# Optimization experiments

Measured on AMD Instinct MI355X. Metric: run time of the kernel, lower is better.

The kernel has to match this reference:

```python
import jax, jax.numpy as jnp
import numpy as np

B, T, V, E, U = 256, 512, 20000, 128, 128


def setup_inputs() -> dict:
    key = jax.random.key(0)
    k = jax.random.split(key, 7)
    tokens = jax.random.randint(k[0], (B, T), 0, V)
    emb_table = jax.random.normal(k[1], (V, E), jnp.float32) * 0.05
    kernel = jax.random.normal(k[2], (E, 4 * U), jnp.float32) * 0.05
    recurrent_kernel = jax.random.normal(k[3], (U, 4 * U), jnp.float32) * 0.05
    # Keras default: unit_forget_bias -> forget-gate bias = 1, others 0 (gate order i,f,c,o)
    bias = jnp.concatenate([jnp.zeros(U), jnp.ones(U), jnp.zeros(2 * U)]).astype(jnp.float32)
    dense_w = jax.random.normal(k[4], (U, 1), jnp.float32) * 0.05
    dense_b = jnp.zeros((1,), jnp.float32)
    return {"tokens": tokens, "emb_table": emb_table, "kernel": kernel,
            "recurrent_kernel": recurrent_kernel, "bias": bias,
            "dense_w": dense_w, "dense_b": dense_b}


def reference(tokens, emb_table, kernel, recurrent_kernel, bias, dense_w, dense_b):
    # Embedding lookup: [B,T] -> [B,T,E]
    x = emb_table[tokens]
    # Precompute input projections for all timesteps: [B,T,4U]
    zx = jnp.einsum('bte,eg->btg', x, kernel) + bias

    def step(carry, z_t):
        h, c = carry
        z = z_t + h @ recurrent_kernel          # [B,4U]
        i, f, g, o = jnp.split(z, 4, axis=-1)   # Keras gate order i,f,c,o
        i = jax.nn.sigmoid(i)
        f = jax.nn.sigmoid(f)
        g = jnp.tanh(g)
        o = jax.nn.sigmoid(o)
        c = f * c + i * g
        h = o * jnp.tanh(c)
        return (h, c), None

    h0 = jnp.zeros((tokens.shape[0], U), zx.dtype)
    c0 = jnp.zeros((tokens.shape[0], U), zx.dtype)
    (h_final, _), _ = jax.lax.scan(step, (h0, c0), jnp.swapaxes(zx, 0, 1))
    # Dense sigmoid head: [B,1]
    return jax.nn.sigmoid(h_final @ dense_w + dense_b)
```

## Files before the change

### kernel.cpp

```cpp
#include <hip/hip_runtime.h>
#include <hip/hip_bf16.h>

#define BB 256
#define TT 512
#define VV 20000
#define EE 128
#define UU 128
#define G4 512

typedef _Float16 h2 __attribute__((ext_vector_type(2)));

__device__ __forceinline__ float sigmoid_f(float x) {
    float e = __expf(-x);
    return __builtin_amdgcn_rcpf(1.0f + e);
}
__device__ __forceinline__ float tanh_f(float x) {
    float e = __expf(2.0f * x);
    return 1.0f - 2.0f * __builtin_amdgcn_rcpf(e + 1.0f);
}

__device__ __forceinline__ int dpp_i(int v, int pat) {
    switch (pat) {
        case 0xB1: return __builtin_amdgcn_mov_dpp(v, 0xB1, 0xF, 0xF, true);
        case 0x4E: return __builtin_amdgcn_mov_dpp(v, 0x4E, 0xF, 0xF, true);
        case 0x00: return __builtin_amdgcn_mov_dpp(v, 0x00, 0xF, 0xF, true);
        case 0x55: return __builtin_amdgcn_mov_dpp(v, 0x55, 0xF, 0xF, true);
        case 0xAA: return __builtin_amdgcn_mov_dpp(v, 0xAA, 0xF, 0xF, true);
        default:   return __builtin_amdgcn_mov_dpp(v, 0xFF, 0xF, 0xF, true);
    }
}
__device__ __forceinline__ float dpp_f(float v, int pat) {
    return __int_as_float(dpp_i(__float_as_int(v), pat));
}
__device__ __forceinline__ h2 pk_add_dpp(h2 s, int pat) {
    int m = dpp_i(__builtin_bit_cast(int, s), pat);
    return s + __builtin_bit_cast(h2, m);
}

__global__ __launch_bounds__(512, 2) void proj_kernel(
    const float* __restrict__ emb, const float* __restrict__ wk,
    const float* __restrict__ bias, float* __restrict__ P2) {
    const int tid = threadIdx.x;
    const int g   = tid & 3;
    const int u   = tid >> 2;
    const int col = g * 128 + u;
    const int v0  = blockIdx.x * 16;

    __shared__ float elds[16 * EE];
    ((float4*)elds)[tid] = ((const float4*)(emb + (size_t)v0 * EE))[tid];
    __syncthreads();

    float bcol = bias[col];
    float acc[16];
#pragma unroll
    for (int r = 0; r < 16; ++r) acc[r] = bcol;

    const float4* elds4 = (const float4*)elds;
    for (int e0 = 0; e0 < EE; e0 += 4) {
        float k0 = wk[(e0 + 0) * G4 + col];
        float k1 = wk[(e0 + 1) * G4 + col];
        float k2 = wk[(e0 + 2) * G4 + col];
        float k3 = wk[(e0 + 3) * G4 + col];
#pragma unroll
        for (int r = 0; r < 16; ++r) {
            float4 ev = elds4[r * 32 + (e0 >> 2)];
            acc[r] = fmaf(ev.x, k0, acc[r]);
            acc[r] = fmaf(ev.y, k1, acc[r]);
            acc[r] = fmaf(ev.z, k2, acc[r]);
            acc[r] = fmaf(ev.w, k3, acc[r]);
        }
    }
#pragma unroll
    for (int r = 0; r < 16; ++r)
        P2[(size_t)(v0 + r) * G4 + tid] = acc[r];
}

__global__ __launch_bounds__(512) __attribute__((amdgpu_waves_per_eu(2, 2)))
void lstm_kernel(
    const int* __restrict__ tokens, const float* __restrict__ rk,
    const float* __restrict__ P2, const float* __restrict__ dense_w,
    const float* __restrict__ dense_b, float* __restrict__ out) {
    const int tid = threadIdx.x;
    const int u   = tid >> 2;
    const int q   = tid & 3;
    const int b   = blockIdx.x;

    __shared__ __align__(16) _Float16 hh[2][UU];
    __shared__ int   tokLDS[TT + 4];
    __shared__ float red[8];

    h2 wgt[4][16];
    const float* rkb = rk + (size_t)(32 * q) * G4;
#pragma unroll
    for (int g = 0; g < 4; ++g) {
        const int c = g * 128 + u;
#pragma unroll
        for (int p = 0; p < 16; ++p) {
            h2 hw;
            hw.x = (_Float16)rkb[(2 * p + 0) * G4 + c];
            hw.y = (_Float16)rkb[(2 * p + 1) * G4 + c];
            wgt[g][p] = hw;
        }
    }

    const int* trow = tokens + (size_t)b * TT;
    tokLDS[tid] = trow[tid];
    if (tid < 4) tokLDS[TT + tid] = trow[TT - 1];
    if (tid < UU) hh[0][tid] = (_Float16)0.f;

    const int pOff = 4 * u + q;
    float c_state = 0.f, hv = 0.f;
    float pf0 = P2[(size_t)trow[0] * G4 + pOff];
    float pf1 = P2[(size_t)trow[1] * G4 + pOff];
    __syncthreads();

    const h2 zzero = {(_Float16)0.f, (_Float16)0.f};

#define LSTEP(PAR, PF)                                                        \
    {                                                                         \
        int vtok = tokLDS[t + (PAR) + 2];                                     \
        float pcur = (PF);                               \
        (PF) = P2[(size_t)vtok * G4 + pOff];          \
        const int4* hrow = (const int4*)&hh[PAR][32 * q];                     \
        int4 hA = hrow[0], hB = hrow[1], hC = hrow[2], hD = hrow[3];          \
        h2 hr[16];                                                            \
        hr[0]  = __builtin_bit_cast(h2, hA.x);                                \
        hr[1]  = __builtin_bit_cast(h2, hA.y);                                \
        hr[2]  = __builtin_bit_cast(h2, hA.z);                                \
        hr[3]  = __builtin_bit_cast(h2, hA.w);                                \
        hr[4]  = __builtin_bit_cast(h2, hB.x);                                \
        hr[5]  = __builtin_bit_cast(h2, hB.y);                                \
        hr[6]  = __builtin_bit_cast(h2, hB.z);                                \
        hr[7]  = __builtin_bit_cast(h2, hB.w);                                \
        hr[8]  = __builtin_bit_cast(h2, hC.x);                                \
        hr[9]  = __builtin_bit_cast(h2, hC.y);                                \
        hr[10] = __builtin_bit_cast(h2, hC.z);                                \
        hr[11] = __builtin_bit_cast(h2, hC.w);                                \
        hr[12] = __builtin_bit_cast(h2, hD.x);                                \
        hr[13] = __builtin_bit_cast(h2, hD.y);                                \
        hr[14] = __builtin_bit_cast(h2, hD.z);                                \
        hr[15] = __builtin_bit_cast(h2, hD.w);                                \
              \
        h2 a0[4], a1[4];                                                      \
        _Pragma("unroll")                                                     \
        for (int g = 0; g < 4; ++g) { a0[g] = zzero; a1[g] = zzero; }         \
        _Pragma("unroll")                                                     \
        for (int p = 0; p < 16; p += 2) {                                     \
            _Pragma("unroll")                                                 \
            for (int g = 0; g < 4; ++g) {                                     \
                a0[g] = hr[p] * wgt[g][p] + a0[g];                            \
                a1[g] = hr[p + 1] * wgt[g][p + 1] + a1[g];                    \
            }                                                                 \
        }                                                                     \
         \
        h2 s0 = a0[0] + a1[0], s1 = a0[1] + a1[1];                            \
        h2 s2 = a0[2] + a1[2], s3 = a0[3] + a1[3];                            \
        s0 = pk_add_dpp(s0, 0xB1); s0 = pk_add_dpp(s0, 0x4E);                 \
        s1 = pk_add_dpp(s1, 0xB1); s1 = pk_add_dpp(s1, 0x4E);                 \
        s2 = pk_add_dpp(s2, 0xB1); s2 = pk_add_dpp(s2, 0x4E);                 \
        s3 = pk_add_dpp(s3, 0xB1); s3 = pk_add_dpp(s3, 0x4E);                 \
                 \
        int ilo = (q & 1) ? __builtin_bit_cast(int, s1)                       \
                          : __builtin_bit_cast(int, s0);                      \
        int ihi = (q & 1) ? __builtin_bit_cast(int, s3)                       \
                          : __builtin_bit_cast(int, s2);                      \
        h2 own  = __builtin_bit_cast(h2, (q & 2) ? ihi : ilo);                \
        float zq = (float)own.x + (float)own.y + pcur;                        \
        float xs = (q == 2) ? zq + zq : zq;                                   \
        float sg = sigmoid_f(xs);                                             \
        float av = (q == 2) ? fmaf(2.f, sg, -1.f) : sg;                       \
                                     \
        float ai = dpp_f(av, 0x00);                                           \
        float af_ = dpp_f(av, 0x55);                                          \
        float ag = dpp_f(av, 0xAA);                                           \
        float ao = dpp_f(av, 0xFF);                                           \
        c_state = fmaf(af_, c_state, ai * ag);                                \
        hv      = ao * tanh_f(c_state);                                       \
        if (q == 0) hh[(PAR) ^ 1][u] = (_Float16)hv;                          \
        asm volatile("s_waitcnt lgkmcnt(0)" ::: "memory");                    \
        __builtin_amdgcn_s_barrier();                                         \
    }

    for (int t = 0; t < TT; t += 2) {
        LSTEP(0, pf0)
        LSTEP(1, pf1)
    }
#undef LSTEP

    float val = (q == 0) ? hv * dense_w[u] : 0.f;
#pragma unroll
    for (int off = 32; off > 0; off >>= 1) val += __shfl_xor(val, off, 64);
    if ((tid & 63) == 0) red[tid >> 6] = val;
    __syncthreads();
    if (tid == 0) {
        float s = dense_b[0];
#pragma unroll
        for (int i = 0; i < 8; ++i) s += red[i];
        out[b] = sigmoid_f(s);
    }
}

extern "C" void kernel_launch(void* const* d_in, const int* in_sizes, int n_in,
                              void* d_out, int out_size, void* d_ws, size_t ws_size,
                              hipStream_t stream) {
    const int*   tokens = (const int*)  d_in[0];
    const float* emb    = (const float*)d_in[1];
    const float* wk     = (const float*)d_in[2];
    const float* rk     = (const float*)d_in[3];
    const float* bias   = (const float*)d_in[4];
    const float* dw     = (const float*)d_in[5];
    const float* db     = (const float*)d_in[6];
    float* out = (float*)d_out;
    float* P2  = (float*)d_ws;

    proj_kernel<<<VV / 16, 512, 0, stream>>>(emb, wk, bias, P2);
    lstm_kernel<<<BB, 512, 0, stream>>>(tokens, rk, P2, dw, db, out);
}
```

Baseline: 355.9 us.

## Give each thread a full K-column per gate, removing cross-lane DPP reduction

Repartitions the recurrent matvec so each thread owns all 128 input rows for its own gate column instead of a 32-row slice across all four gates. This removes the per-step DPP butterfly reduction and gate selection, replacing them with a local tree of packed fp16 adds, and uses inline-asm v_pk_fma_f16. In exchange each thread reads the entire h vector from LDS every step, four times more LDS traffic, and accumulates longer fp16 chains, which may affect precision.

```diff
diff --git a/kernel.cpp b/kernel.cpp
--- a/kernel.cpp
+++ b/kernel.cpp
@@ -19,22 +19,25 @@
     return 1.0f - 2.0f * __builtin_amdgcn_rcpf(e + 1.0f);
 }
 
-__device__ __forceinline__ int dpp_i(int v, int pat) {
+__device__ __forceinline__ h2 pk_fma(h2 a, h2 b, h2 c) {
+    int d, ia = __builtin_bit_cast(int, a), ib = __builtin_bit_cast(int, b),
+        ic = __builtin_bit_cast(int, c);
+    asm("v_pk_fma_f16 %0, %1, %2, %3" : "=v"(d) : "v"(ia), "v"(ib), "v"(ic));
+    return __builtin_bit_cast(h2, d);
+}
+__device__ __forceinline__ h2 pk_add(h2 a, h2 b) {
+    int d, ia = __builtin_bit_cast(int, a), ib = __builtin_bit_cast(int, b);
+    asm("v_pk_add_f16 %0, %1, %2" : "=v"(d) : "v"(ia), "v"(ib));
+    return __builtin_bit_cast(h2, d);
+}
+
+__device__ __forceinline__ float dpp_f(float v, int pat) {
     switch (pat) {
-        case 0xB1: return __builtin_amdgcn_mov_dpp(v, 0xB1, 0xF, 0xF, true);
-        case 0x4E: return __builtin_amdgcn_mov_dpp(v, 0x4E, 0xF, 0xF, true);
-        case 0x00: return __builtin_amdgcn_mov_dpp(v, 0x00, 0xF, 0xF, true);
-        case 0x55: return __builtin_amdgcn_mov_dpp(v, 0x55, 0xF, 0xF, true);
-        case 0xAA: return __builtin_amdgcn_mov_dpp(v, 0xAA, 0xF, 0xF, true);
-        default:   return __builtin_amdgcn_mov_dpp(v, 0xFF, 0xF, 0xF, true);
+        case 0x00: return __int_as_float(__builtin_amdgcn_mov_dpp(__float_as_int(v), 0x00, 0xF, 0xF, true));
+        case 0x55: return __int_as_float(__builtin_amdgcn_mov_dpp(__float_as_int(v), 0x55, 0xF, 0xF, true));
+        case 0xAA: return __int_as_float(__builtin_amdgcn_mov_dpp(__float_as_int(v), 0xAA, 0xF, 0xF, true));
+        default:   return __int_as_float(__builtin_amdgcn_mov_dpp(__float_as_int(v), 0xFF, 0xF, 0xF, true));
     }
-}
-__device__ __forceinline__ float dpp_f(float v, int pat) {
-    return __int_as_float(dpp_i(__float_as_int(v), pat));
-}
-__device__ __forceinline__ h2 pk_add_dpp(h2 s, int pat) {
-    int m = dpp_i(__builtin_bit_cast(int, s), pat);
-    return s + __builtin_bit_cast(h2, m);
 }
 
 __global__ __launch_bounds__(512, 2) void proj_kernel(
@@ -89,17 +92,15 @@
     __shared__ int   tokLDS[TT + 4];
     __shared__ float red[8];
 
-    h2 wgt[4][16];
-    const float* rkb = rk + (size_t)(32 * q) * G4;
+    h2 wgt[64];
+    {
+        const int c = q * 128 + u;
 #pragma unroll
-    for (int g = 0; g < 4; ++g) {
-        const int c = g * 128 + u;
-#pragma unroll
-        for (int p = 0; p < 16; ++p) {
+        for (int p = 0; p < 64; ++p) {
             h2 hw;
-            hw.x = (_Float16)rkb[(2 * p + 0) * G4 + c];
-            hw.y = (_Float16)rkb[(2 * p + 1) * G4 + c];
-            wgt[g][p] = hw;
+            hw.x = (_Float16)rk[(size_t)(2 * p + 0) * G4 + c];
+            hw.y = (_Float16)rk[(size_t)(2 * p + 1) * G4 + c];
+            wgt[p] = hw;
         }
     }
 
@@ -108,10 +109,10 @@
     if (tid < 4) tokLDS[TT + tid] = trow[TT - 1];
     if (tid < UU) hh[0][tid] = (_Float16)0.f;
 
-    const int pOff = 4 * u + q;
+    const float* Pcol = P2 + (size_t)(4 * u + q);
     float c_state = 0.f, hv = 0.f;
-    float pf0 = P2[(size_t)trow[0] * G4 + pOff];
-    float pf1 = P2[(size_t)trow[1] * G4 + pOff];
+    float pf0 = Pcol[(size_t)trow[0] * G4];
+    float pf1 = Pcol[(size_t)trow[1] * G4];
     __syncthreads();
 
     const h2 zzero = {(_Float16)0.f, (_Float16)0.f};
@@ -120,60 +121,40 @@
     {                                                                         \
         int vtok = tokLDS[t + (PAR) + 2];                                     \
         float pcur = (PF);                               \
-        (PF) = P2[(size_t)vtok * G4 + pOff];          \
-        const int4* hrow = (const int4*)&hh[PAR][32 * q];                     \
-        int4 hA = hrow[0], hB = hrow[1], hC = hrow[2], hD = hrow[3];          \
-        h2 hr[16];                                                            \
-        hr[0]  = __builtin_bit_cast(h2, hA.x);                                \
-        hr[1]  = __builtin_bit_cast(h2, hA.y);                                \
-        hr[2]  = __builtin_bit_cast(h2, hA.z);                                \
-        hr[3]  = __builtin_bit_cast(h2, hA.w);                                \
-        hr[4]  = __builtin_bit_cast(h2, hB.x);                                \
-        hr[5]  = __builtin_bit_cast(h2, hB.y);                                \
-        hr[6]  = __builtin_bit_cast(h2, hB.z);                                \
-        hr[7]  = __builtin_bit_cast(h2, hB.w);                                \
-        hr[8]  = __builtin_bit_cast(h2, hC.x);                                \
-        hr[9]  = __builtin_bit_cast(h2, hC.y);                                \
-        hr[10] = __builtin_bit_cast(h2, hC.z);                                \
-        hr[11] = __builtin_bit_cast(h2, hC.w);                                \
-        hr[12] = __builtin_bit_cast(h2, hD.x);                                \
-        hr[13] = __builtin_bit_cast(h2, hD.y);                                \
-        hr[14] = __builtin_bit_cast(h2, hD.z);                                \
-        hr[15] = __builtin_bit_cast(h2, hD.w);                                \
-              \
-        h2 a0[4], a1[4];                                                      \
+        (PF) = Pcol[(size_t)vtok * G4];               \
+                             \
+        const int4* hp = (const int4*)&hh[PAR][0];                            \
+        int4 hw_[16];                                                         \
         _Pragma("unroll")                                                     \
-        for (int g = 0; g < 4; ++g) { a0[g] = zzero; a1[g] = zzero; }         \
+        for (int r = 0; r < 16; ++r) hw_[r] = hp[r];                          \
+                          \
+        h2 acc[8];                                                            \
         _Pragma("unroll")                                                     \
-        for (int p = 0; p < 16; p += 2) {                                     \
+        for (int c = 0; c < 8; ++c) acc[c] = zzero;                           \
+        _Pragma("unroll")                                                     \
+        for (int i = 0; i < 8; ++i) {                                         \
             _Pragma("unroll")                                                 \
-            for (int g = 0; g < 4; ++g) {                                     \
-                a0[g] = hr[p] * wgt[g][p] + a0[g];                            \
-                a1[g] = hr[p + 1] * wgt[g][p + 1] + a1[g];                    \
+            for (int c = 0; c < 8; ++c) {                                     \
+                int pi = i * 8 + c;                                           \
+                h2 hval = __builtin_bit_cast(h2, (&hw_[0].x)[pi * 4 / 4]);    \
+                acc[c] = pk_fma(hval, wgt[pi], acc[c]);                       \
             }                                                                 \
         }                                                                     \
-         \
-        h2 s0 = a0[0] + a1[0], s1 = a0[1] + a1[1];                            \
-        h2 s2 = a0[2] + a1[2], s3 = a0[3] + a1[3];                            \
-        s0 = pk_add_dpp(s0, 0xB1); s0 = pk_add_dpp(s0, 0x4E);                 \
-        s1 = pk_add_dpp(s1, 0xB1); s1 = pk_add_dpp(s1, 0x4E);                 \
-        s2 = pk_add_dpp(s2, 0xB1); s2 = pk_add_dpp(s2, 0x4E);                 \
-        s3 = pk_add_dpp(s3, 0xB1); s3 = pk_add_dpp(s3, 0x4E);                 \
-                 \
-        int ilo = (q & 1) ? __builtin_bit_cast(int, s1)                       \
-                          : __builtin_bit_cast(int, s0);                      \
-        int ihi = (q & 1) ? __builtin_bit_cast(int, s3)                       \
-                          : __builtin_bit_cast(int, s2);                      \
-        h2 own  = __builtin_bit_cast(h2, (q & 2) ? ihi : ilo);                \
-        float zq = (float)own.x + (float)own.y + pcur;                        \
+                                   \
+        h2 s01 = pk_add(acc[0], acc[1]), s23 = pk_add(acc[2], acc[3]);        \
+        h2 s45 = pk_add(acc[4], acc[5]), s67 = pk_add(acc[6], acc[7]);        \
+        h2 s03 = pk_add(s01, s23), s47 = pk_add(s45, s67);                    \
+        h2 sAll = pk_add(s03, s47);                                           \
+        float zq = (float)sAll.x + (float)sAll.y + pcur;                      \
+                   \
         float xs = (q == 2) ? zq + zq : zq;                                   \
         float sg = sigmoid_f(xs);                                             \
         float av = (q == 2) ? fmaf(2.f, sg, -1.f) : sg;                       \
-                                     \
-        float ai = dpp_f(av, 0x00);                                           \
+                                             \
+        float ai  = dpp_f(av, 0x00);                                          \
         float af_ = dpp_f(av, 0x55);                                          \
-        float ag = dpp_f(av, 0xAA);                                           \
-        float ao = dpp_f(av, 0xFF);                                           \
+        float ag  = dpp_f(av, 0xAA);                                          \
+        float ao  = dpp_f(av, 0xFF);                                          \
         c_state = fmaf(af_, c_state, ai * ag);                                \
         hv      = ao * tanh_f(c_state);                                       \
         if (q == 0) hh[(PAR) ^ 1][u] = (_Float16)hv;                          \
```

Result: slower. 372.9 us (+4.8%).
